# Optimization experiments

Measured on AMD Instinct MI355X. Metric: run time of the kernel, lower is better.

## Reference

```python
import jax, jax.numpy as jnp
import numpy as np

# 7 axial hex directions (dy, dx) including center, matching HexConv2d.DIRS
DIRS = [(0, 0), (1, 0), (0, 1), (-1, 1), (-1, 0), (0, -1), (1, -1)]


def _shift(x, dy, dx):
    """torch.roll-style shift with zero fill at wrapped edges. x: [B,C,H,W]."""
    sx, sy = -dx, -dy
    y = jnp.roll(x, shift=(sy, sx), axis=(2, 3))
    if sy > 0:
        y = y.at[:, :, :sy, :].set(0)
    elif sy < 0:
        y = y.at[:, :, sy:, :].set(0)
    if sx > 0:
        y = y.at[:, :, :, :sx].set(0)
    elif sx < 0:
        y = y.at[:, :, :, sx:].set(0)
    return y


def _hex_mask(H, dtype):
    size = H // 2
    q = jnp.arange(-size, size + 1)
    Q, R = jnp.meshgrid(q, q, indexing='ij')
    S = -Q - R
    # |Q|<=size and |R|<=size hold by construction; only |S|<=size cuts corners
    mask = ((jnp.abs(Q) <= size) & (jnp.abs(R) <= size) & (jnp.abs(S) <= size))
    return mask.astype(dtype)[None, None]  # [1,1,H,W]


def setup_inputs() -> dict:
    key = jax.random.key(0)
    k1, k2, k3 = jax.random.split(key, 3)
    B, Cin, Cout, H = 32, 256, 256, 49
    x = jax.random.normal(k1, (B, Cin, H, H), dtype=jnp.float32)
    weight = jax.random.normal(k2, (Cout, Cin, 7), dtype=jnp.float32) * 0.02
    bias = jax.random.normal(k3, (Cout,), dtype=jnp.float32) * 0.02
    return {"x": x, "weight": weight, "bias": bias}


def reference(x, weight, bias):
    mask = _hex_mask(x.shape[2], x.dtype)          # [1,1,H,W]
    x = x * mask
    # [7,B,C,H,W]: shifted+masked neighbor maps
    nbr = jnp.stack([_shift(x, dy, dx) for (dy, dx) in DIRS], axis=0) * mask
    # fused 1x1 conv over (channel, direction): weight [O,C,7]
    y = jnp.einsum('nbchw,ocn->bohw', nbr, weight) + bias[None, :, None, None]
    return y * mask
```

## Files before the change

kernel.cpp:

```cpp
#include <hip/hip_runtime.h>


typedef __attribute__((ext_vector_type(8))) short short8;
typedef __attribute__((ext_vector_type(4))) short short4v;
typedef __attribute__((ext_vector_type(4))) float floatx4;

#define NPIX   2401
#define W50    50
#define PREAL  2450
#define XBLEAD 56
#define XBROWS 2672
#define PT11   80
#define NT11   32
#define NSEG11 12
#define KCOL11 (NSEG11*1024)
#define BUF11  (2*KCOL11)
#define XB3_BYTES ((size_t)32*XBROWS*256*2)
#define WP_BYTES  917504ULL
#define WS_NEED3  (XB3_BYTES + WP_BYTES)
#define NPADROW 271

#define X4_BLKS 4864
#define Z_BLKS  1084
#define W_BLKS  224
#define PREP_BLKS (X4_BLKS + Z_BLKS + W_BLKS)

__device__ __forceinline__ unsigned short f2bf(float f) {
  unsigned u = __builtin_bit_cast(unsigned, f);
  u += 0x7fffu + ((u >> 16) & 1u);
  return (unsigned short)(u >> 16);
}

__device__ __forceinline__ void prep_w_body(const float* __restrict__ w,
                                            unsigned short* __restrict__ wp, int tt) {
  int l  = tt & 63;
  int ot = (tt >> 6) & 15;
  int kc = (tt >> 10) & 7;
  int n  = tt >> 13;
  int o  = ot * 16 + (l & 15);
  int cb = kc * 32 + ((l >> 4) * 8);
  const float* src = w + (size_t)(o * 256 + cb) * 7 + n;
  short8 pk;
#pragma unroll
  for (int j = 0; j < 8; ++j) pk[j] = (short)f2bf(src[j * 7]);
  ((short8*)wp)[tt] = pk;
}

__global__ __launch_bounds__(256)
void prep_all(const float* __restrict__ x, const float* __restrict__ w,
              unsigned short* __restrict__ xb, unsigned short* __restrict__ wp) {
  __shared__ unsigned short t[64][68];
  const int tid = threadIdx.x;
  const int blk = blockIdx.x;

  if (blk < X4_BLKS) {
    const int l = blk;
    const int span = l % 38, cg = (l / 38) & 3, b = l / 152;
    const int s0 = span * 64;
    {
      const int chl = tid >> 2, i4 = tid & 3;
      const float* src = x + ((size_t)(b * 256 + cg * 64 + chl)) * NPIX;
      const int rbase = s0 + i4 * 16;
#pragma unroll
      for (int it = 0; it < 4; ++it) {
        int r = rbase + it * 4;
        float vv[4] = {0.f, 0.f, 0.f, 0.f};
        if (r + 3 < NPIX) {
          float4 v = *(const float4*)(src + r);
          vv[0] = v.x; vv[1] = v.y; vv[2] = v.z; vv[3] = v.w;
        } else {
#pragma unroll
          for (int e = 0; e < 4; ++e) if (r + e < NPIX) vv[e] = src[r + e];
        }
        short4v u = {0, 0, 0, 0};
#pragma unroll
        for (int e = 0; e < 4; ++e) {
          int re = r + e;
          unsigned short uu = 0;
          if (re < NPIX) {
            int h = re / 49, ww = re - h * 49, s = h + ww;
            if (s >= 24 && s <= 72) uu = f2bf(vv[e]);
          }
          u[e] = (short)uu;
        }
        *(short4v*)&t[chl][i4 * 16 + it * 4] = u;
      }
    }
    __syncthreads();
    const int pp = tid >> 3;
    const int co = tid & 7;
    unsigned d[8];
#pragma unroll
    for (int k = 0; k < 8; ++k) d[k] = *(const unsigned*)&t[co * 8 + k][pp * 2];
    uint4 lo, hi;
    {
      unsigned l0[4], h0[4];
#pragma unroll
      for (int m = 0; m < 4; ++m) {
        unsigned a = d[2 * m], bq = d[2 * m + 1];
        l0[m] = (a & 0xffffu) | (bq << 16);
        h0[m] = (a >> 16) | (bq & 0xffff0000u);
      }
      lo = make_uint4(l0[0], l0[1], l0[2], l0[3]);
      hi = make_uint4(h0[0], h0[1], h0[2], h0[3]);
    }
    const int r_lo = s0 + pp * 2, r_hi = r_lo + 1;
    if (r_lo < NPIX) {
      int prow = r_lo + r_lo / 49 + XBLEAD;
      *(uint4*)(xb + ((size_t)b * XBROWS + prow) * 256 + cg * 64 + co * 8) = lo;
    }
    if (r_hi < NPIX) {
      int prow = r_hi + r_hi / 49 + XBLEAD;
      *(uint4*)(xb + ((size_t)b * XBROWS + prow) * 256 + cg * 64 + co * 8) = hi;
    }
  } else if (blk < X4_BLKS + Z_BLKS) {
    int idx = (blk - X4_BLKS) * 256 + tid;
    if (idx >= 32 * NPADROW * 32) return;
    int c16 = idx & 31;
    int rr  = idx >> 5;
    int pr  = rr % NPADROW;
    int b   = rr / NPADROW;
    int row;
    if (pr < 56)        row = pr;
    else if (pr < 105)  row = 105 + 50 * (pr - 56);
    else                row = 2506 + (pr - 105);
    short8 z = {0,0,0,0,0,0,0,0};
    *(short8*)(xb + ((size_t)b * XBROWS + row) * 256 + c16 * 8) = z;
  } else {
    prep_w_body(w, wp, (blk - X4_BLKS - Z_BLKS) * 256 + tid);
  }
}

__global__ void prep_w_kernel(const float* __restrict__ w, unsigned short* __restrict__ wp) {
  prep_w_body(w, wp, blockIdx.x * 256 + threadIdx.x);
}

__global__ __launch_bounds__(256, 3)
void hexconv_v11(const unsigned short* __restrict__ xb,
                 const unsigned short* __restrict__ wp,
                 const float* __restrict__ bias,
                 float* __restrict__ out) {
  __shared__ __attribute__((aligned(16))) unsigned char smem[2 * BUF11];

  const int tid  = threadIdx.x;
  const int lane = tid & 63;
  const int wv   = tid >> 6;
  const int col  = lane & 15;
  const int quad = lane >> 4;

  const int bx = blockIdx.x;
  const int pt = (bx & 7) * 4 + (bx >> 3);
  const int b  = blockIdx.y;
  const int P0 = pt * PT11;
  const int phase = ((pt + b) & 3) * 2;

  const int OFF[7] = {0, 50, 1, -49, -50, -1, 49};

  int ba[7];
#pragma unroll
  for (int n = 0; n < 7; ++n) {
    int r0 = col + 56 + OFF[n];
    int r64 = r0 << 6;
    ba[n] = (r64 + quad * 16) ^ ((r64 >> 3) & 0x30);
  }

  const int gpart = (lane & 3) ^ ((lane >> 3) & 3);
  const char* gsrc0 = (const char*)(xb + ((size_t)b * XBROWS + (size_t)P0) * 256)
                      + (lane >> 2) * 512 + gpart * 16;

  auto stage2 = [&](int buf, int kc0) {
    char* ldsb = (char*)smem + buf * BUF11;
    for (int u = wv; u < 2 * NSEG11; u += 4) {
      int kk = (u >= NSEG11) ? 1 : 0;
      int s  = u - kk * NSEG11;
      __builtin_amdgcn_global_load_lds(
          (const __attribute__((address_space(1))) unsigned int*)
              (gsrc0 + (size_t)s * 8192 + (kc0 + kk) * 64),
          (__attribute__((address_space(3))) unsigned int*)(ldsb + u * 1024), 16, 0, 0);
    }
  };

  const char* wbase = (const char*)wp + (size_t)(wv * 4) * 1024 + lane * 16;

  floatx4 acc[4][5];
#pragma unroll
  for (int ii = 0; ii < 4; ++ii)
#pragma unroll
    for (int j = 0; j < 5; ++j) acc[ii][j] = (floatx4){0.f, 0.f, 0.f, 0.f};

  stage2(0, phase);
  __syncthreads();

  for (int i = 0; i < 4; ++i) {
    const int kc0  = (2 * i + phase) & 7;
    const int kc0n = (2 * i + 2 + phase) & 7;
    if (i < 3) stage2((i + 1) & 1, kc0n);
    const char* bufp = (const char*)smem + (i & 1) * BUF11;
#pragma unroll
    for (int n = 0; n < 7; ++n) {
#pragma unroll
      for (int kk = 0; kk < 2; ++kk) {
        const int kc = kc0 + kk;
        short8 af[4];
#pragma unroll
        for (int ii = 0; ii < 4; ++ii)
          af[ii] = *(const short8*)(wbase + ((size_t)((n * 8 + kc) * 16 + ii)) * 1024);
        const char* bp = bufp + kk * KCOL11 + ba[n];
        short8 bfv[5];
#pragma unroll
        for (int j = 0; j < 5; ++j)
          bfv[j] = *(const short8*)(bp + j * 1024);
        __builtin_amdgcn_s_setprio(1);
#pragma unroll
        for (int j = 0; j < 5; ++j)
#pragma unroll
          for (int ii = 0; ii < 4; ++ii)
            acc[ii][j] = __builtin_amdgcn_mfma_f32_16x16x32_bf16(af[ii], bfv[j], acc[ii][j], 0, 0, 0);
        __builtin_amdgcn_s_setprio(0);
      }
    }
    if (i < 3) __syncthreads();
  }

  const int ob = wv * 64;
#pragma unroll
  for (int ii = 0; ii < 4; ++ii) {
    floatx4 bv = *(const floatx4*)(bias + ob + ii * 16 + quad * 4);
#pragma unroll
    for (int j = 0; j < 5; ++j)
#pragma unroll
      for (int rr = 0; rr < 4; ++rr) acc[ii][j][rr] += bv[rr];
  }

#pragma unroll
  for (int j = 0; j < 5; ++j) {
    int p = P0 + j * 16 + col;
    int h = p / W50;
    int w = p - h * W50;
    if (w >= 49 || p >= PREAL) continue;
    bool m = (h + w >= 24) && (h + w <= 72);
    int ridx = h * 49 + w;
#pragma unroll
    for (int ii = 0; ii < 4; ++ii) {
      float* dst = out + ((b * 256 + ob + ii * 16 + quad * 4) * NPIX + ridx);
#pragma unroll
      for (int rr = 0; rr < 4; ++rr) {
        float v = m ? acc[ii][j][rr] : 0.f;
        dst[rr * NPIX] = v;
      }
    }
  }
}

#define PITCH  40
#define V1WIN  168
#define V1ZROW 168
__global__ __launch_bounds__(256)
void hexconv_v1(const float* __restrict__ x,
                const unsigned short* __restrict__ wp,
                const float* __restrict__ bias,
                float* __restrict__ out) {
  __shared__ unsigned short sm[(V1ZROW + 2) * PITCH];
  const int tid = threadIdx.x, lane = tid & 63, wv = tid >> 6;
  const int col = lane & 15, quad = lane >> 4;
  const int pt = blockIdx.x, b = blockIdx.y;
  const int P0 = pt * 64, win_start = P0 - 52;
  if (tid < PITCH * 2) sm[V1ZROW * PITCH + tid] = 0;
  const int OFF[7] = {0, 49, 1, -48, -49, -1, 48};
  const int DXP = (1 << 2) | (1 << 3), DXN = (1 << 5) | (1 << 6);
  int baddr[4][7];
#pragma unroll
  for (int j = 0; j < 4; ++j) {
    int pix = P0 + j * 16 + col;
    int wj = pix % 49;
    int rowbase = pix - win_start;
#pragma unroll
    for (int n = 0; n < 7; ++n) {
      bool bad = (((DXP >> n) & 1) && wj == 48) || (((DXN >> n) & 1) && wj == 0);
      int row = bad ? V1ZROW : (rowbase + OFF[n]);
      baddr[j][n] = row * (PITCH * 2) + quad * 16;
    }
  }
  int sp[3], sgp[3]; bool sok[3];
#pragma unroll
  for (int pi = 0; pi < 3; ++pi) {
    int p = lane + pi * 64, gp = win_start + p;
    sp[pi] = p; sgp[pi] = gp;
    bool hm = false;
    if (gp >= 0 && gp < NPIX) { int h = gp / 49, w = gp - h * 49, s = h + w; hm = (s >= 24 && s <= 72); }
    sok[pi] = (p < V1WIN) && hm;
  }
  floatx4 acc[4][4];
#pragma unroll
  for (int i = 0; i < 4; ++i)
#pragma unroll
    for (int j = 0; j < 4; ++j) acc[i][j] = (floatx4){0.f, 0.f, 0.f, 0.f};
  const short8* wpv = (const short8*)wp;
  const int wslot = wv * 4;
  for (int kc = 0; kc < 8; ++kc) {
    __syncthreads();
#pragma unroll
    for (int ci = 0; ci < 8; ++ci) {
      int c = ci * 4 + wv;
      const float* src = x + ((size_t)(b * 256 + kc * 32 + c)) * NPIX;
#pragma unroll
      for (int pi = 0; pi < 3; ++pi) {
        if (sp[pi] < V1WIN) {
          float v = sok[pi] ? src[sgp[pi]] : 0.f;
          sm[sp[pi] * PITCH + c] = f2bf(v);
        }
      }
    }
    __syncthreads();
#pragma unroll
    for (int n = 0; n < 7; ++n) {
      short8 af[4];
#pragma unroll
      for (int i = 0; i < 4; ++i)
        af[i] = wpv[((size_t)((n * 8 + kc) * 16 + wslot + i)) * 64 + lane];
      short8 bf[4];
#pragma unroll
      for (int j = 0; j < 4; ++j)
        bf[j] = *(const short8*)((const char*)sm + baddr[j][n]);
#pragma unroll
      for (int i = 0; i < 4; ++i)
#pragma unroll
        for (int j = 0; j < 4; ++j)
          acc[i][j] = __builtin_amdgcn_mfma_f32_16x16x32_bf16(af[i], bf[j], acc[i][j], 0, 0, 0);
    }
  }
  const int ob = wv * 64;
  floatx4 bv[4];
#pragma unroll
  for (int i = 0; i < 4; ++i)
    bv[i] = *(const floatx4*)(bias + ob + i * 16 + quad * 4);
#pragma unroll
  for (int j = 0; j < 4; ++j) {
    int pix = P0 + j * 16 + col;
    if (pix >= NPIX) continue;
    int h = pix / 49, w = pix - h * 49;
    bool m = (h + w >= 24 && h + w <= 72);
#pragma unroll
    for (int i = 0; i < 4; ++i) {
      int o = ob + i * 16 + quad * 4;
      float* dst = out + ((size_t)(b * 256 + o)) * NPIX + pix;
#pragma unroll
      for (int r = 0; r < 4; ++r) {
        float v = m ? (acc[i][j][r] + bv[i][r]) : 0.f;
        dst[(size_t)r * NPIX] = v;
      }
    }
  }
}

extern "C" void kernel_launch(void* const* d_in, const int* in_sizes, int n_in,
                              void* d_out, int out_size, void* d_ws, size_t ws_size,
                              hipStream_t stream) {
  const float* x    = (const float*)d_in[0];
  const float* w    = (const float*)d_in[1];
  const float* bias = (const float*)d_in[2];
  float* out = (float*)d_out;

  if (ws_size >= WS_NEED3) {
    unsigned short* xb = (unsigned short*)d_ws;
    unsigned short* wp = (unsigned short*)((char*)d_ws + XB3_BYTES);
    prep_all<<<PREP_BLKS, 256, 0, stream>>>(x, w, xb, wp);
    hexconv_v11<<<dim3(NT11, 32), 256, 0, stream>>>(xb, wp, bias, out);
  } else {
    unsigned short* wp = (unsigned short*)d_ws;
    prep_w_kernel<<<224, 256, 0, stream>>>(w, wp);
    hexconv_v1<<<dim3(38, 32), 256, 0, stream>>>(x, wp, bias, out);
  }
}
```

Measured before the change: 233.2 us.

## Split output channels across two blocks and stage one K-chunk per buffer

Each block now covers 128 output channels instead of 256, so the grid doubles to 64x32 and each wave accumulates a 2x5 tile rather than 4x5. The LDS staging buffer holds a single K-chunk per stage (half the previous size) and the main loop runs 8 iterations instead of 4, with the launch bound raised to 4 blocks per CU. The aim is more resident waves and smaller LDS and register footprints to hide latency. The cost is that the activation tile is now loaded twice (once per output half) and there are more barriers, with fewer MFMAs per LDS read.

Measured after the change: 236.9 us. Within noise of the previous version (+1.6%).

```diff
diff --git a/kernel.cpp b/kernel.cpp
--- a/kernel.cpp
+++ b/kernel.cpp
@@ -10,11 +10,10 @@
 #define PREAL  2450
 #define XBLEAD 56
 #define XBROWS 2672
-#define PT11   80
-#define NT11   32
-#define NSEG11 12
-#define KCOL11 (NSEG11*1024)
-#define BUF11  (2*KCOL11)
+#define PT12   80
+#define NT12   32
+#define NSEG12 12
+#define BUF12  (NSEG12*1024)
 #define XB3_BYTES ((size_t)32*XBROWS*256*2)
 #define WP_BYTES  917504ULL
 #define WS_NEED3  (XB3_BYTES + WP_BYTES)
@@ -135,12 +134,12 @@
   prep_w_body(w, wp, blockIdx.x * 256 + threadIdx.x);
 }
 
-__global__ __launch_bounds__(256, 3)
-void hexconv_v11(const unsigned short* __restrict__ xb,
+__global__ __launch_bounds__(256, 4)
+void hexconv_v12(const unsigned short* __restrict__ xb,
                  const unsigned short* __restrict__ wp,
                  const float* __restrict__ bias,
                  float* __restrict__ out) {
-  __shared__ __attribute__((aligned(16))) unsigned char smem[2 * BUF11];
+  __shared__ __attribute__((aligned(16))) unsigned char smem[2 * BUF12];
 
   const int tid  = threadIdx.x;
   const int lane = tid & 63;
@@ -148,11 +147,13 @@
   const int col  = lane & 15;
   const int quad = lane >> 4;
 
-  const int bx = blockIdx.x;
-  const int pt = (bx & 7) * 4 + (bx >> 3);
-  const int b  = blockIdx.y;
-  const int P0 = pt * PT11;
-  const int phase = ((pt + b) & 3) * 2;
+  const int bx  = blockIdx.x;
+  const int oh  = bx & 1;
+  const int bxp = bx >> 1;
+  const int pt  = (bxp & 7) * 4 + (bxp >> 3);
+  const int b   = blockIdx.y;
+  const int P0  = pt * PT12;
+  const int phase = (pt + b + oh * 4) & 7;
 
   const int OFF[7] = {0, 50, 1, -49, -50, -1, 49};
 
@@ -168,63 +169,56 @@
   const char* gsrc0 = (const char*)(xb + ((size_t)b * XBROWS + (size_t)P0) * 256)
                       + (lane >> 2) * 512 + gpart * 16;
 
-  auto stage2 = [&](int buf, int kc0) {
-    char* ldsb = (char*)smem + buf * BUF11;
-    for (int u = wv; u < 2 * NSEG11; u += 4) {
-      int kk = (u >= NSEG11) ? 1 : 0;
-      int s  = u - kk * NSEG11;
+  auto stage1 = [&](int buf, int kc) {
+    char* ldsb = (char*)smem + buf * BUF12;
+    for (int u = wv; u < NSEG12; u += 4) {
       __builtin_amdgcn_global_load_lds(
           (const __attribute__((address_space(1))) unsigned int*)
-              (gsrc0 + (size_t)s * 8192 + (kc0 + kk) * 64),
+              (gsrc0 + (size_t)u * 8192 + kc * 64),
           (__attribute__((address_space(3))) unsigned int*)(ldsb + u * 1024), 16, 0, 0);
     }
   };
 
-  const char* wbase = (const char*)wp + (size_t)(wv * 4) * 1024 + lane * 16;
-
-  floatx4 acc[4][5];
-#pragma unroll
-  for (int ii = 0; ii < 4; ++ii)
+  const char* wbase = (const char*)wp + (size_t)(oh * 8 + wv * 2) * 1024 + lane * 16;
+
+  floatx4 acc[2][5];
+#pragma unroll
+  for (int ii = 0; ii < 2; ++ii)
 #pragma unroll
     for (int j = 0; j < 5; ++j) acc[ii][j] = (floatx4){0.f, 0.f, 0.f, 0.f};
 
-  stage2(0, phase);
+  stage1(0, phase);
   __syncthreads();
 
-  for (int i = 0; i < 4; ++i) {
-    const int kc0  = (2 * i + phase) & 7;
-    const int kc0n = (2 * i + 2 + phase) & 7;
-    if (i < 3) stage2((i + 1) & 1, kc0n);
-    const char* bufp = (const char*)smem + (i & 1) * BUF11;
+  for (int i = 0; i < 8; ++i) {
+    const int kc = (i + phase) & 7;
+    if (i < 7) stage1((i + 1) & 1, (i + 1 + phase) & 7);
+    const char* bufp = (const char*)smem + (i & 1) * BUF12;
 #pragma unroll
     for (int n = 0; n < 7; ++n) {
-#pragma unroll
-      for (int kk = 0; kk < 2; ++kk) {
-        const int kc = kc0 + kk;
-        short8 af[4];
-#pragma unroll
-        for (int ii = 0; ii < 4; ++ii)
-          af[ii] = *(const short8*)(wbase + ((size_t)((n * 8 + kc) * 16 + ii)) * 1024);
-        const char* bp = bufp + kk * KCOL11 + ba[n];
-        short8 bfv[5];
-#pragma unroll
-        for (int j = 0; j < 5; ++j)
-          bfv[j] = *(const short8*)(bp + j * 1024);
-        __builtin_amdgcn_s_setprio(1);
-#pragma unroll
-        for (int j = 0; j < 5; ++j)
-#pragma unroll
-          for (int ii = 0; ii < 4; ++ii)
-            acc[ii][j] = __builtin_amdgcn_mfma_f32_16x16x32_bf16(af[ii], bfv[j], acc[ii][j], 0, 0, 0);
-        __builtin_amdgcn_s_setprio(0);
-      }
-    }
-    if (i < 3) __syncthreads();
-  }
-
-  const int ob = wv * 64;
-#pragma unroll
-  for (int ii = 0; ii < 4; ++ii) {
+      short8 af[2];
+#pragma unroll
+      for (int ii = 0; ii < 2; ++ii)
+        af[ii] = *(const short8*)(wbase + ((size_t)((n * 8 + kc) * 16 + ii)) * 1024);
+      const char* bp = bufp + ba[n];
+      short8 bfv[5];
+#pragma unroll
+      for (int j = 0; j < 5; ++j)
+        bfv[j] = *(const short8*)(bp + j * 1024);
+      __builtin_amdgcn_s_setprio(1);
+#pragma unroll
+      for (int j = 0; j < 5; ++j)
+#pragma unroll
+        for (int ii = 0; ii < 2; ++ii)
+          acc[ii][j] = __builtin_amdgcn_mfma_f32_16x16x32_bf16(af[ii], bfv[j], acc[ii][j], 0, 0, 0);
+      __builtin_amdgcn_s_setprio(0);
+    }
+    if (i < 7) __syncthreads();
+  }
+
+  const int ob = oh * 128 + wv * 32;
+#pragma unroll
+  for (int ii = 0; ii < 2; ++ii) {
     floatx4 bv = *(const floatx4*)(bias + ob + ii * 16 + quad * 4);
 #pragma unroll
     for (int j = 0; j < 5; ++j)
@@ -241,7 +235,7 @@
     bool m = (h + w >= 24) && (h + w <= 72);
     int ridx = h * 49 + w;
 #pragma unroll
-    for (int ii = 0; ii < 4; ++ii) {
+    for (int ii = 0; ii < 2; ++ii) {
       float* dst = out + ((b * 256 + ob + ii * 16 + quad * 4) * NPIX + ridx);
 #pragma unroll
       for (int rr = 0; rr < 4; ++rr) {
@@ -365,7 +359,7 @@
     unsigned short* xb = (unsigned short*)d_ws;
     unsigned short* wp = (unsigned short*)((char*)d_ws + XB3_BYTES);
     prep_all<<<PREP_BLKS, 256, 0, stream>>>(x, w, xb, wp);
-    hexconv_v11<<<dim3(NT11, 32), 256, 0, stream>>>(xb, wp, bias, out);
+    hexconv_v12<<<dim3(64, 32), 256, 0, stream>>>(xb, wp, bias, out);
   } else {
     unsigned short* wp = (unsigned short*)d_ws;
     prep_w_kernel<<<224, 256, 0, stream>>>(w, wp);
```

## Use triple-buffered single-chunk LDS staging with register-prefetched weight fragments

Applied to the files above, without the earlier changes.

Replaces the double-buffered two-chunk-per-stage pipeline with a three-slot ring that stages one K-chunk at a time, two chunks ahead. Weight fragments for the next direction are prefetched into a ping-pong register set so global weight loads overlap the MFMAs. The phase rotation now covers all 8 chunks instead of 4 pairs, and launch bounds drop from 3 to 2 blocks per SM. The aim is to hide load latency better, at the cost of more barriers, higher register pressure and possibly lower occupancy.

Result: no change. 231.3 us (-0.8%).

```diff
diff --git a/kernel.cpp b/kernel.cpp
--- a/kernel.cpp
+++ b/kernel.cpp
@@ -10,11 +10,9 @@
 #define PREAL  2450
 #define XBLEAD 56
 #define XBROWS 2672
-#define PT11   80
-#define NT11   32
-#define NSEG11 12
-#define KCOL11 (NSEG11*1024)
-#define BUF11  (2*KCOL11)
+#define PT13   80
+#define NSEG13 12
+#define BUF13  (NSEG13*1024)
 #define XB3_BYTES ((size_t)32*XBROWS*256*2)
 #define WP_BYTES  917504ULL
 #define WS_NEED3  (XB3_BYTES + WP_BYTES)
@@ -135,12 +133,49 @@
   prep_w_body(w, wp, blockIdx.x * 256 + threadIdx.x);
 }
 
-__global__ __launch_bounds__(256, 3)
-void hexconv_v11(const unsigned short* __restrict__ xb,
+#define HEX_ITER(IVAL, JPAR, DO_STAGE, DO_PRE_LAST)                           \
+  {                                                                           \
+    const int i_ = (IVAL);                                                    \
+    if (DO_STAGE) stage1((i_ + 2) % 3, (i_ + 2 + phase) & 7);                 \
+    const int kcc_ = (i_ + phase) & 7;                                        \
+    const int kcn_ = (i_ + 1 + phase) & 7;                                    \
+    const char* bufp_ = (const char*)smem + (i_ % 3) * BUF13;                 \
+    _Pragma("unroll")                                                         \
+    for (int n = 0; n < 7; ++n) {                                             \
+      const int cs = (n + (JPAR)) & 1;                                        \
+      const int ns = cs ^ 1;                                                  \
+      if (n < 6) {                                                            \
+        _Pragma("unroll")                                                     \
+        for (int ii = 0; ii < 4; ++ii)                                        \
+          afr[ns][ii] = *(const short8*)(wbase +                              \
+              (size_t)(((n + 1) * 8 + kcc_) * 16 + ii) * 1024);               \
+      } else if (DO_PRE_LAST) {                                               \
+        _Pragma("unroll")                                                     \
+        for (int ii = 0; ii < 4; ++ii)                                        \
+          afr[ns][ii] = *(const short8*)(wbase +                              \
+              (size_t)((kcn_ * 16) + ii) * 1024);                             \
+      }                                                                       \
+      const char* bp_ = bufp_ + ba[n];                                        \
+      short8 bfv[5];                                                          \
+      _Pragma("unroll")                                                       \
+      for (int j = 0; j < 5; ++j) bfv[j] = *(const short8*)(bp_ + j * 1024);  \
+      __builtin_amdgcn_s_setprio(1);                                          \
+      _Pragma("unroll")                                                       \
+      for (int j = 0; j < 5; ++j)                                             \
+        _Pragma("unroll")                                                     \
+        for (int ii = 0; ii < 4; ++ii)                                        \
+          acc[ii][j] = __builtin_amdgcn_mfma_f32_16x16x32_bf16(               \
+              afr[cs][ii], bfv[j], acc[ii][j], 0, 0, 0);                      \
+      __builtin_amdgcn_s_setprio(0);                                          \
+    }                                                                         \
+  }
+
+__global__ __launch_bounds__(256, 2)
+void hexconv_v13(const unsigned short* __restrict__ xb,
                  const unsigned short* __restrict__ wp,
                  const float* __restrict__ bias,
                  float* __restrict__ out) {
-  __shared__ __attribute__((aligned(16))) unsigned char smem[2 * BUF11];
+  __shared__ __attribute__((aligned(16))) unsigned char smem[3 * BUF13];
 
   const int tid  = threadIdx.x;
   const int lane = tid & 63;
@@ -151,8 +186,8 @@
   const int bx = blockIdx.x;
   const int pt = (bx & 7) * 4 + (bx >> 3);
   const int b  = blockIdx.y;
-  const int P0 = pt * PT11;
-  const int phase = ((pt + b) & 3) * 2;
+  const int P0 = pt * PT13;
+  const int phase = (pt + b) & 7;
 
   const int OFF[7] = {0, 50, 1, -49, -50, -1, 49};
 
@@ -168,59 +203,42 @@
   const char* gsrc0 = (const char*)(xb + ((size_t)b * XBROWS + (size_t)P0) * 256)
                       + (lane >> 2) * 512 + gpart * 16;
 
-  auto stage2 = [&](int buf, int kc0) {
-    char* ldsb = (char*)smem + buf * BUF11;
-    for (int u = wv; u < 2 * NSEG11; u += 4) {
-      int kk = (u >= NSEG11) ? 1 : 0;
-      int s  = u - kk * NSEG11;
+  auto stage1 = [&](int slot, int kc) {
+    char* ldsb = (char*)smem + slot * BUF13;
+    for (int u = wv; u < NSEG13; u += 4) {
       __builtin_amdgcn_global_load_lds(
           (const __attribute__((address_space(1))) unsigned int*)
-              (gsrc0 + (size_t)s * 8192 + (kc0 + kk) * 64),
+              (gsrc0 + (size_t)u * 8192 + kc * 64),
           (__attribute__((address_space(3))) unsigned int*)(ldsb + u * 1024), 16, 0, 0);
     }
   };
 
   const char* wbase = (const char*)wp + (size_t)(wv * 4) * 1024 + lane * 16;
 
+  short8 afr[2][4];
   floatx4 acc[4][5];
 #pragma unroll
   for (int ii = 0; ii < 4; ++ii)
 #pragma unroll
     for (int j = 0; j < 5; ++j) acc[ii][j] = (floatx4){0.f, 0.f, 0.f, 0.f};
 
-  stage2(0, phase);
+  stage1(0, phase);
+  stage1(1, (1 + phase) & 7);
+#pragma unroll
+  for (int ii = 0; ii < 4; ++ii)
+    afr[0][ii] = *(const short8*)(wbase + (size_t)((phase * 16) + ii) * 1024);
   __syncthreads();
 
-  for (int i = 0; i < 4; ++i) {
-    const int kc0  = (2 * i + phase) & 7;
-    const int kc0n = (2 * i + 2 + phase) & 7;
-    if (i < 3) stage2((i + 1) & 1, kc0n);
-    const char* bufp = (const char*)smem + (i & 1) * BUF11;
-#pragma unroll
-    for (int n = 0; n < 7; ++n) {
-#pragma unroll
-      for (int kk = 0; kk < 2; ++kk) {
-        const int kc = kc0 + kk;
-        short8 af[4];
-#pragma unroll
-        for (int ii = 0; ii < 4; ++ii)
-          af[ii] = *(const short8*)(wbase + ((size_t)((n * 8 + kc) * 16 + ii)) * 1024);
-        const char* bp = bufp + kk * KCOL11 + ba[n];
-        short8 bfv[5];
-#pragma unroll
-        for (int j = 0; j < 5; ++j)
-          bfv[j] = *(const short8*)(bp + j * 1024);
-        __builtin_amdgcn_s_setprio(1);
-#pragma unroll
-        for (int j = 0; j < 5; ++j)
-#pragma unroll
-          for (int ii = 0; ii < 4; ++ii)
-            acc[ii][j] = __builtin_amdgcn_mfma_f32_16x16x32_bf16(af[ii], bfv[j], acc[ii][j], 0, 0, 0);
-        __builtin_amdgcn_s_setprio(0);
-      }
-    }
-    if (i < 3) __syncthreads();
-  }
+#pragma unroll 1
+  for (int p = 0; p < 3; ++p) {
+    HEX_ITER(2 * p,     0, true, true);
+    __syncthreads();
+    HEX_ITER(2 * p + 1, 1, true, true);
+    __syncthreads();
+  }
+  HEX_ITER(6, 0, false, true);
+  __syncthreads();
+  HEX_ITER(7, 1, false, false);
 
   const int ob = wv * 64;
 #pragma unroll
@@ -365,7 +383,7 @@
     unsigned short* xb = (unsigned short*)d_ws;
     unsigned short* wp = (unsigned short*)((char*)d_ws + XB3_BYTES);
     prep_all<<<PREP_BLKS, 256, 0, stream>>>(x, w, xb, wp);
-    hexconv_v11<<<dim3(NT11, 32), 256, 0, stream>>>(xb, wp, bias, out);
+    hexconv_v13<<<dim3(32, 32), 256, 0, stream>>>(xb, wp, bias, out);
   } else {
     unsigned short* wp = (unsigned short*)d_ws;
     prep_w_kernel<<<224, 256, 0, stream>>>(w, wp);
```
